# Kernel optimization log

Measured on AMD Instinct MI355X. Metric: run time of the kernel, lower is better.

Reference implementation:

```python
import jax, jax.numpy as jnp
import numpy as np

B, L, C, H = 8, 2048, 512, 8
HD = C // H
MLP_H = int(C * 4.0)
LN_EPS = 1e-5


def _dwconv(x, w, b, groups):
    # x: (B, C, L), w: (C, C//groups, 3), 'same' padding depthwise/grouped conv
    y = jax.lax.conv_general_dilated(
        x, w, window_strides=(1,), padding=((1, 1),),
        feature_group_count=groups,
        dimension_numbers=('NCH', 'OIH', 'NCH'))
    return y + b[None, :, None]


def _ln(x, g, b):
    mu = x.mean(-1, keepdims=True)
    var = ((x - mu) ** 2).mean(-1, keepdims=True)
    return (x - mu) * jax.lax.rsqrt(var + LN_EPS) * g + b


def setup_inputs() -> dict:
    key = jax.random.key(0)
    ks = jax.random.split(key, 32)
    s = 0.02
    d = {
        'x_q': jax.random.normal(ks[0], (B, L, C), jnp.float32),
        'x_kv': jax.random.normal(ks[1], (B, L, C), jnp.float32),
        'cpe1_w': jax.random.normal(ks[2], (C, 1, 3), jnp.float32) * s,
        'cpe1_b': jnp.zeros((C,), jnp.float32),
        'norm1_g': jnp.ones((C,), jnp.float32),
        'norm1_b': jnp.zeros((C,), jnp.float32),
        'in_w': jax.random.normal(ks[3], (C, C), jnp.float32) * s,
        'in_b': jnp.zeros((C,), jnp.float32),
        'act_w': jax.random.normal(ks[4], (C, C), jnp.float32) * s,
        'act_b': jnp.zeros((C,), jnp.float32),
        'dwc_w': jax.random.normal(ks[5], (C, 1, 3), jnp.float32) * s,
        'dwc_b': jnp.zeros((C,), jnp.float32),
        'q_w': jax.random.normal(ks[6], (C, C), jnp.float32) * s,
        'q_b': jnp.zeros((C,), jnp.float32),
        'kv_w': jax.random.normal(ks[7], (C, 2 * C), jnp.float32) * s,
        'kv_b': jnp.zeros((2 * C,), jnp.float32),
        'lepe_w': jax.random.normal(ks[8], (C, 1, 3), jnp.float32) * s,
        'lepe_b': jnp.zeros((C,), jnp.float32),
        'out_w': jax.random.normal(ks[9], (C, C), jnp.float32) * s,
        'out_b': jnp.zeros((C,), jnp.float32),
        'cpe2_w': jax.random.normal(ks[10], (C, 1, 3), jnp.float32) * s,
        'cpe2_b': jnp.zeros((C,), jnp.float32),
        'norm2_g': jnp.ones((C,), jnp.float32),
        'norm2_b': jnp.zeros((C,), jnp.float32),
        'fc1_w': jax.random.normal(ks[11], (C, MLP_H), jnp.float32) * s,
        'fc1_b': jnp.zeros((MLP_H,), jnp.float32),
        'fc2_w': jax.random.normal(ks[12], (MLP_H, C), jnp.float32) * s,
        'fc2_b': jnp.zeros((C,), jnp.float32),
    }
    return d


def _linear_attention(x_q, x_kv, q_w, q_b, kv_w, kv_b, lepe_w, lepe_b):
    b, n, c = x_kv.shape
    kv = x_kv @ kv_w + kv_b                       # (b, n, 2c)
    k, v = kv[..., :c], kv[..., c:]
    q = jax.nn.elu(x_q @ q_w + q_b) + 1.0
    k = jax.nn.elu(k) + 1.0
    # (b, h, n, d)
    q = q.reshape(b, n, H, HD).transpose(0, 2, 1, 3)
    k = k.reshape(b, n, H, HD).transpose(0, 2, 1, 3)
    v = v.reshape(b, n, H, HD).transpose(0, 2, 1, 3)
    k_mean = k.mean(axis=2)                       # (b, h, d)
    z = 1.0 / (jnp.einsum('bhnd,bhd->bhn', q, k_mean) + 1e-6)
    scale = n ** (-0.5)
    kv_mat = jnp.einsum('bhnd,bhne->bhde', k * scale, v * scale)  # (b,h,d,d)
    out = jnp.einsum('bhnd,bhde->bhne', q, kv_mat) * z[..., None]
    out = out.transpose(0, 2, 1, 3).reshape(b, n, c)
    v_flat = v.transpose(0, 2, 1, 3).reshape(b, n, c).transpose(0, 2, 1)  # (b,c,n)
    out = out + _dwconv(v_flat, lepe_w, lepe_b, groups=c).transpose(0, 2, 1)
    return out


def reference(x_q, x_kv, cpe1_w, cpe1_b, norm1_g, norm1_b, in_w, in_b, act_w,
              act_b, dwc_w, dwc_b, q_w, q_b, kv_w, kv_b, lepe_w, lepe_b,
              out_w, out_b, cpe2_w, cpe2_b, norm2_g, norm2_b, fc1_w, fc1_b,
              fc2_w, fc2_b):
    b, l, c = x_kv.shape
    x = x_kv + _dwconv(x_kv.transpose(0, 2, 1), cpe1_w, cpe1_b, c).transpose(0, 2, 1)
    shortcut = x
    x = _ln(x, norm1_g, norm1_b)
    act_res = jax.nn.silu(x @ act_w + act_b)
    # NOTE: torch uses .view(B, C, L): a reshape, not a transpose -- replicate faithfully
    xp = (x @ in_w + in_b).reshape(b, c, l)
    xp = jax.nn.silu(_dwconv(xp, dwc_w, dwc_b, c)).reshape(b, l, c)
    xa = _linear_attention(x_q, xp, q_w, q_b, kv_w, kv_b, lepe_w, lepe_b)
    x = shortcut + ((xa * act_res) @ out_w + out_b)
    x = x + _dwconv(x.transpose(0, 2, 1), cpe2_w, cpe2_b, c).transpose(0, 2, 1)
    h = _ln(x, norm2_g, norm2_b)
    h = jax.nn.gelu(h @ fc1_w + fc1_b, approximate=False) @ fc2_w + fc2_b
    return x + h
```

## Files before the change

kernel.cpp:

```cpp
#include <hip/hip_runtime.h>
#include <cmath>


typedef __bf16 bf16;
typedef __bf16 bf16x8 __attribute__((ext_vector_type(8)));
typedef __bf16 bf16x4 __attribute__((ext_vector_type(4)));
typedef float  f32x4  __attribute__((ext_vector_type(4)));

#define B_  8
#define L_  2048
#define C_  512
#define M_  (B_ * L_)

__device__ __forceinline__ float fastrcp(float x) { return __builtin_amdgcn_rcpf(x); }

__device__ __forceinline__ float siluf(float x)
{
    return x * fastrcp(1.f + __expf(-x));
}
__device__ __forceinline__ float elu1f(float x) { return x > 0.f ? x + 1.f : __expf(x); }

__device__ __forceinline__ float geluf(float x)
{
    const float z = fabsf(x) * 0.70710678118654752f;
    const float t = fastrcp(__builtin_fmaf(z, 0.47047f, 1.f));
    const float poly = t * (0.3480242f + t * (-0.0958798f + t * 0.7478556f));
    const float erfz = __builtin_fmaf(-poly, __expf(-z * z), 1.f);
    const float hx = 0.5f * x;
    return __builtin_fmaf(hx, __builtin_copysignf(erfz, x), hx);
}

__device__ __forceinline__ void load_lds16(const bf16* g, bf16* l)
{
    __builtin_amdgcn_global_load_lds(
        (const __attribute__((address_space(1))) void*)g,
        (__attribute__((address_space(3))) void*)l, 16, 0, 0);
}

__global__ __launch_bounds__(256) void zero_k(float* __restrict__ p, int n)
{
    int i = blockIdx.x * 256 + threadIdx.x;
    if (i < n) p[i] = 0.f;
}

__global__ __launch_bounds__(64) void ws_diag_k(float* __restrict__ out, float v)
{
    if (threadIdx.x == 0 && blockIdx.x == 0) out[0] = v;
}

__global__ __launch_bounds__(256) void f32_to_bf16_k(
    const float* __restrict__ in, bf16* __restrict__ out, int n4)
{
    int i = blockIdx.x * 256 + threadIdx.x;
    if (i >= n4) return;
    float4 v = ((const float4*)in)[i];
    bf16x4 o = { (bf16)v.x, (bf16)v.y, (bf16)v.z, (bf16)v.w };
    ((bf16x4*)out)[i] = o;
}

struct TJob  { const float* W; bf16* Wt; int K; int N; int blk0; };
struct TJobs { TJob j[7]; };

__global__ __launch_bounds__(256) void transpose_all_k(TJobs jobs)
{
    __shared__ float tile[32][33];
    const int bid = blockIdx.x;
    int ji = 0;
#pragma unroll
    for (int i = 1; i < 7; ++i) if (bid >= jobs.j[i].blk0) ji = i;
    const float* W  = jobs.j[ji].W;
    bf16*        Wt = jobs.j[ji].Wt;
    const int K = jobs.j[ji].K, N = jobs.j[ji].N;
    const int rel = bid - jobs.j[ji].blk0;
    const int nb = N >> 5;
    const int n0 = (rel % nb) * 32, k0 = (rel / nb) * 32;
    const int tx = threadIdx.x & 31, ty = threadIdx.x >> 5;
#pragma unroll
    for (int i = 0; i < 32; i += 8)
        tile[ty + i][tx] = W[(size_t)(k0 + ty + i) * N + n0 + tx];
    __syncthreads();
#pragma unroll
    for (int i = 0; i < 32; i += 8)
        Wt[(size_t)(n0 + ty + i) * K + k0 + tx] = (bf16)tile[tx][ty + i];
}

__global__ __launch_bounds__(256) void cpe_ln_k(
    const float* __restrict__ xin, const float* __restrict__ cw,
    const float* __restrict__ cb, const float* __restrict__ g,
    const float* __restrict__ bb, float* __restrict__ xres,
    bf16* __restrict__ xln)
{
    const int token = blockIdx.x;
    const int l = token & (L_ - 1);
    const int tid = threadIdx.x;
    const float* row = xin + (size_t)token * C_;
    float v[2]; float s = 0.f, s2 = 0.f;
#pragma unroll
    for (int i = 0; i < 2; ++i) {
        const int c = tid + i * 256;
        float x0 = row[c];
        float xm = (l > 0)      ? row[c - C_] : 0.f;
        float xp = (l < L_ - 1) ? row[c + C_] : 0.f;
        float t = x0 + xm * cw[3*c] + x0 * cw[3*c+1] + xp * cw[3*c+2] + cb[c];
        v[i] = t; s += t; s2 += t * t;
    }
#pragma unroll
    for (int off = 32; off; off >>= 1) { s += __shfl_down(s, off); s2 += __shfl_down(s2, off); }
    __shared__ float rs[4], rs2[4];
    if ((tid & 63) == 0) { rs[tid >> 6] = s; rs2[tid >> 6] = s2; }
    __syncthreads();
    s  = rs[0] + rs[1] + rs[2] + rs[3];
    s2 = rs2[0] + rs2[1] + rs2[2] + rs2[3];
    const float mu = s * (1.f / C_);
    const float rstd = rsqrtf(s2 * (1.f / C_) - mu * mu + 1e-5f);
    float* orow = xres + (size_t)token * C_;
    bf16*  lrow = xln  + (size_t)token * C_;
#pragma unroll
    for (int i = 0; i < 2; ++i) {
        const int c = tid + i * 256;
        orow[c] = v[i];
        lrow[c] = (bf16)((v[i] - mu) * rstd * g[c] + bb[c]);
    }
}

__global__ __launch_bounds__(256) void dwc_silu_k(
    const bf16* __restrict__ Y, const float* __restrict__ w,
    const float* __restrict__ b, bf16* __restrict__ xp)
{
    const size_t idx = (size_t)blockIdx.x * 256 + threadIdx.x;
    const int m = (int)(idx & (size_t)(L_ * C_ - 1));
    const int ch = m >> 11;
    const int pos = m & (L_ - 1);
    float x0 = (float)Y[idx];
    float xm = (pos > 0)      ? (float)Y[idx - 1] : 0.f;
    float xq = (pos < L_ - 1) ? (float)Y[idx + 1] : 0.f;
    float t = xm * w[3*ch] + x0 * w[3*ch+1] + xq * w[3*ch+2] + b[ch];
    xp[idx] = (bf16)siluf(t);
}

__global__ __launch_bounds__(256) void ksum_k(
    const bf16* __restrict__ kvbT, float* __restrict__ ksum)
{
    const int c = blockIdx.x;
    const int wave = threadIdx.x >> 6, lane = threadIdx.x & 63;
#pragma unroll
    for (int i = 0; i < 2; ++i) {
        const int b = wave + i * 4;
        const bf16* src = kvbT + (size_t)c * M_ + b * L_ + lane * 32;
        float s = 0.f;
#pragma unroll
        for (int u = 0; u < 4; ++u) {
            bf16x8 v = *(const bf16x8*)(src + u * 8);
#pragma unroll
            for (int j = 0; j < 8; ++j) s += (float)v[j];
        }
#pragma unroll
        for (int o = 32; o; o >>= 1) s += __shfl_down(s, o);
        if (lane == 0) ksum[b * C_ + c] = s;
    }
}

__global__ __launch_bounds__(256) void kvmat_mfma_k(
    const bf16* __restrict__ kvbT, float* __restrict__ kvpart)
{
    const int bh = blockIdx.x, b = bh >> 3, h = bh & 7;
    const int tid = threadIdx.x;
    const int wave = tid >> 6, lane = tid & 63;
    const int l16 = lane & 15, quad = lane >> 4;
    __shared__ bf16 As[64 * 72];
    __shared__ bf16 Bs[64 * 72];
    const int r = tid >> 2;
    const int cseg = (tid & 3) * 16;
    const size_t kRow = (size_t)(h * 64 + r) * M_;
    const size_t vRow = (size_t)(512 + h * 64 + r) * M_;

    f32x4 acc[4];
    const f32x4 z4 = { 0.f, 0.f, 0.f, 0.f };
#pragma unroll
    for (int ni = 0; ni < 4; ++ni) acc[ni] = z4;

    for (int it = 0; it < 8; ++it) {
        const size_t colBase = (size_t)b * L_ + blockIdx.y * 512 + it * 64;
        {
            const bf16* ga = kvbT + vRow + colBase + cseg;
            const bf16* gb = kvbT + kRow + colBase + cseg;
            *(uint4*)&As[r * 72 + cseg]     = *(const uint4*)ga;
            *(uint4*)&As[r * 72 + cseg + 8] = *(const uint4*)(ga + 8);
            *(uint4*)&Bs[r * 72 + cseg]     = *(const uint4*)gb;
            *(uint4*)&Bs[r * 72 + cseg + 8] = *(const uint4*)(gb + 8);
        }
        __syncthreads();
#pragma unroll
        for (int kk = 0; kk < 64; kk += 32) {
            bf16x8 af = *(const bf16x8*)(&As[(wave * 16 + l16) * 72 + kk + quad * 8]);
#pragma unroll
            for (int ni = 0; ni < 4; ++ni) {
                bf16x8 bfr = *(const bf16x8*)(&Bs[(ni * 16 + l16) * 72 + kk + quad * 8]);
                acc[ni] = __builtin_amdgcn_mfma_f32_16x16x32_bf16(af, bfr, acc[ni], 0, 0, 0);
            }
        }
        __syncthreads();
    }
    float* dst = kvpart + (size_t)blockIdx.y * 262144 + (size_t)bh * 4096;
#pragma unroll
    for (int ni = 0; ni < 4; ++ni)
#pragma unroll
        for (int rr = 0; rr < 4; ++rr)
            dst[(wave * 16 + quad * 4 + rr) * 64 + ni * 16 + l16] = acc[ni][rr];
}

__global__ __launch_bounds__(256) void kvconv_k(
    const float* __restrict__ p, bf16* __restrict__ out)
{
    int i = blockIdx.x * 256 + threadIdx.x;
    float s = p[i] + p[i + 262144] + p[i + 2 * 262144] + p[i + 3 * 262144];
    out[i] = (bf16)(s * (1.f / (float)L_));
}

__global__ __launch_bounds__(256) void attn_mfma_k(
    const bf16* __restrict__ q, const bf16* __restrict__ kvbT,
    const bf16* __restrict__ kvmatT, const float* __restrict__ ksum,
    const float* __restrict__ lw, const float* __restrict__ lb,
    const bf16* __restrict__ act_res, bf16* __restrict__ xa_mul)
{
    const int bh = blockIdx.x, b = bh >> 3, h = bh & 7;
    const int n0 = blockIdx.y * 64;
    const int tid = threadIdx.x;
    const int wave = tid >> 6, lane = tid & 63;
    const int l16 = lane & 15, quad = lane >> 4;

    __shared__ bf16 kvT[64 * 72];
    __shared__ bf16 kmS[64];

#pragma unroll
    for (int i = 0; i < 2; ++i) {
        const int idx = i * 256 + tid;
        const int row = idx >> 3, col = (idx & 7) * 8;
        *(bf16x8*)&kvT[row * 72 + col] =
            *(const bf16x8*)&kvmatT[(size_t)bh * 4096 + idx * 8];
    }
    if (tid < 64) kmS[tid] = (bf16)(ksum[b * C_ + h * 64 + tid] * (1.f / (float)L_));
    __syncthreads();

    const int tok = n0 + wave * 16;
    const bf16* qbase = q + ((size_t)b * L_ + tok) * C_ + h * 64;
    const bf16x8 af0 = *(const bf16x8*)(qbase + (size_t)l16 * C_ + quad * 8);
    const bf16x8 af1 = *(const bf16x8*)(qbase + (size_t)l16 * C_ + 32 + quad * 8);

    const bf16x8 z8 = { bf16(0.f), bf16(0.f), bf16(0.f), bf16(0.f),
                        bf16(0.f), bf16(0.f), bf16(0.f), bf16(0.f) };
    const bf16x8 km0 = *(const bf16x8*)&kmS[quad * 8];
    const bf16x8 km1 = *(const bf16x8*)&kmS[32 + quad * 8];
    const bf16x8 b20 = (l16 == 0) ? km0 : z8;
    const bf16x8 b21 = (l16 == 0) ? km1 : z8;
    f32x4 zd = { 0.f, 0.f, 0.f, 0.f };
    zd = __builtin_amdgcn_mfma_f32_16x16x32_bf16(af0, b20, zd, 0, 0, 0);
    zd = __builtin_amdgcn_mfma_f32_16x16x32_bf16(af1, b21, zd, 0, 0, 0);
    float zr[4];
#pragma unroll
    for (int r = 0; r < 4; ++r)
        zr[r] = fastrcp(__shfl(zd[r], (lane & 48)) + 1e-6f);

    f32x4 acc[4];
    const f32x4 zf4 = { 0.f, 0.f, 0.f, 0.f };
#pragma unroll
    for (int ni = 0; ni < 4; ++ni) acc[ni] = zf4;
#pragma unroll
    for (int ni = 0; ni < 4; ++ni) {
        const bf16x8 b0 = *(const bf16x8*)&kvT[(ni * 16 + l16) * 72 + quad * 8];
        const bf16x8 b1 = *(const bf16x8*)&kvT[(ni * 16 + l16) * 72 + 32 + quad * 8];
        acc[ni] = __builtin_amdgcn_mfma_f32_16x16x32_bf16(af0, b0, acc[ni], 0, 0, 0);
        acc[ni] = __builtin_amdgcn_mfma_f32_16x16x32_bf16(af1, b1, acc[ni], 0, 0, 0);
    }

#pragma unroll
    for (int ni = 0; ni < 4; ++ni) {
        const int e = ni * 16 + l16;
        const int c = h * 64 + e;
        const float w0 = lw[3*c], w1 = lw[3*c+1], w2 = lw[3*c+2], lbc = lb[c];
        const bf16* vrow = kvbT + (size_t)(512 + c) * M_ + b * L_;
#pragma unroll
        for (int r = 0; r < 4; ++r) {
            const int n = tok + quad * 4 + r;
            const float v0 = (float)vrow[n];
            const float vm = (n > 0)      ? (float)vrow[n - 1] : 0.f;
            const float vp = (n < L_ - 1) ? (float)vrow[n + 1] : 0.f;
            const float lepe = vm * w0 + v0 * w1 + vp * w2 + lbc;
            const float xa = acc[ni][r] * zr[r] + lepe;
            const size_t off = ((size_t)b * L_ + n) * C_ + c;
            xa_mul[off] = (bf16)(xa * (float)act_res[off]);
        }
    }
}

template <int EPI>
__global__ __launch_bounds__(256) void gemm_bt(
    const bf16* __restrict__ A, const bf16* __restrict__ Bt,
    const float* __restrict__ bias, const float* __restrict__ res,
    void* __restrict__ outp, void* __restrict__ outp2, int K, int N)
{
    __shared__ bf16 smem[2 * 128 * 64];
    bf16* As = smem;
    bf16* Bs = smem + 8192;
    const int tid = threadIdx.x;
    const int wave = tid >> 6, lane = tid & 63;
    const int wm = (wave & 1) * 64, wn = (wave >> 1) * 64;
    const int l16 = lane & 15, quad = lane >> 4;
    const size_t tileM = (size_t)blockIdx.x * 128;
    const size_t tileN = (size_t)blockIdx.y * 128;

    const int lrow = lane >> 3;
    const int lcol = (((lane & 7) ^ (lrow & 7))) * 8;
    const int swz  = l16 & 7;

    const f32x4 z4 = { 0.f, 0.f, 0.f, 0.f };
    f32x4 acc[4][4];
#pragma unroll
    for (int mi = 0; mi < 4; ++mi)
#pragma unroll
        for (int ni = 0; ni < 4; ++ni) acc[mi][ni] = z4;

    for (int k0 = 0; k0 < K; k0 += 64) {
#pragma unroll
        for (int it = 0; it < 4; ++it) {
            const int rg = it * 32 + wave * 8;
            load_lds16(A  + (tileM + rg + lrow) * (size_t)K + k0 + lcol, As + rg * 64);
            load_lds16(Bt + (tileN + rg + lrow) * (size_t)K + k0 + lcol, Bs + rg * 64);
        }
        __syncthreads();
#pragma unroll
        for (int kk = 0; kk < 64; kk += 32) {
            bf16x8 af[4], bfr[4];
#pragma unroll
            for (int mi = 0; mi < 4; ++mi)
                af[mi] = *(const bf16x8*)(&As[(wm + mi * 16 + l16) * 64
                                              + ((((kk >> 3) + quad) ^ swz) * 8)]);
#pragma unroll
            for (int ni = 0; ni < 4; ++ni)
                bfr[ni] = *(const bf16x8*)(&Bs[(wn + ni * 16 + l16) * 64
                                               + ((((kk >> 3) + quad) ^ swz) * 8)]);
#pragma unroll
            for (int mi = 0; mi < 4; ++mi)
#pragma unroll
                for (int ni = 0; ni < 4; ++ni)
                    acc[mi][ni] = __builtin_amdgcn_mfma_f32_16x16x32_bf16(
                        af[mi], bfr[ni], acc[mi][ni], 0, 0, 0);
        }
        __syncthreads();
    }

    const int rrow = lane >> 2;
    const int rseg = (lane & 3) * 16;

    if (EPI == 5 || EPI == 7) {
        float* sc = (float*)smem + wave * 1088;
#pragma unroll
        for (int mi = 0; mi < 4; ++mi) {
#pragma unroll
            for (int ni = 0; ni < 4; ++ni)
#pragma unroll
                for (int r = 0; r < 4; ++r)
                    sc[(quad * 4 + r) * 68 + ni * 16 + l16] = acc[mi][ni][r];
            __builtin_amdgcn_sched_barrier(0);
            const size_t rowg = tileM + wm + mi * 16 + rrow;
            const int    colg = (int)tileN + wn + rseg;
            if (EPI == 5) {
                const float* rp = res + rowg * (size_t)N + colg;
                float*       op = (float*)outp + rowg * (size_t)N + colg;
#pragma unroll
                for (int u = 0; u < 4; ++u) {
                    f32x4 v = *(f32x4*)&sc[rrow * 68 + rseg + u * 4];
                    f32x4 rv = *(const f32x4*)(rp + u * 4);
                    f32x4 bv = *(const f32x4*)(bias + colg + u * 4);
                    f32x4 o;
#pragma unroll
                    for (int j = 0; j < 4; ++j) o[j] = v[j] + bv[j] + rv[j];
                    *(f32x4*)(op + u * 4) = o;
                }
            } else {
                const float bv = bias[(int)rowg];
                const bool k_side = (rowg < 512);
                bf16* op = (bf16*)outp + rowg * (size_t)N + colg;
#pragma unroll
                for (int hh = 0; hh < 2; ++hh) {
                    bf16x8 o8;
#pragma unroll
                    for (int j = 0; j < 8; ++j) {
                        float x = sc[rrow * 68 + rseg + hh * 8 + j] + bv;
                        o8[j] = (bf16)(k_side ? elu1f(x) : x);
                    }
                    *(bf16x8*)(op + hh * 8) = o8;
                }
            }
            __builtin_amdgcn_sched_barrier(0);
        }
    } else {
        bf16* sc = (bf16*)smem + wave * 1152;
        float addc[4];
        bool  act_on[4];
#pragma unroll
        for (int ni = 0; ni < 4; ++ni) {
            const int cw = (int)tileN + wn + ni * 16 + l16;
            if (EPI == 8) {
                act_on[ni] = (cw < 512);
                addc[ni] = act_on[ni] ? bias[cw] : res[cw - 512];
            } else { addc[ni] = bias[cw]; act_on[ni] = true; }
        }
#pragma unroll
        for (int mi = 0; mi < 4; ++mi) {
#pragma unroll
            for (int ni = 0; ni < 4; ++ni)
#pragma unroll
                for (int r = 0; r < 4; ++r) {
                    float x = acc[mi][ni][r] + addc[ni];
                    float y;
                    if (EPI == 2)      y = elu1f(x);
                    else if (EPI == 4) y = geluf(x);
                    else               y = act_on[ni] ? siluf(x) : x;
                    sc[(quad * 4 + r) * 72 + ni * 16 + l16] = (bf16)y;
                }
            __builtin_amdgcn_sched_barrier(0);
            const size_t rowg = tileM + wm + mi * 16 + rrow;
            const int    colg = (int)tileN + wn + rseg;
            bf16x8 o0 = *(bf16x8*)&sc[rrow * 72 + rseg];
            bf16x8 o1 = *(bf16x8*)&sc[rrow * 72 + rseg + 8];
            if (EPI == 8) {
                const size_t orow = rowg * (size_t)512;
                bf16* dst = (colg < 512) ? ((bf16*)outp  + orow + colg)
                                         : ((bf16*)outp2 + orow + colg - 512);
                *(bf16x8*)dst = o0; *(bf16x8*)(dst + 8) = o1;
            } else {
                bf16* dst = (bf16*)outp + rowg * (size_t)N + colg;
                *(bf16x8*)dst = o0; *(bf16x8*)(dst + 8) = o1;
            }
            __builtin_amdgcn_sched_barrier(0);
        }
    }
}

template <int EPI>
__global__ __launch_bounds__(512, 2) void gemm8(
    const bf16* __restrict__ A, const bf16* __restrict__ Bt,
    const float* __restrict__ bias, const float* __restrict__ res,
    void* __restrict__ outp, void* __restrict__ outp2, int K, int N)
{
    __shared__ bf16 smem[4 * 256 * 64];
    bf16* const AsBase = smem;
    bf16* const BsBase = smem + 32768;
    const int tid  = threadIdx.x;
    const int wave = tid >> 6, lane = tid & 63;
    const int wrow = wave >> 2, wcol = wave & 3;
    const int l16 = lane & 15, quad = lane >> 4;
    const int lrow = lane >> 3;
    const int lcol = ((lane & 7) ^ lrow) * 8;
    const int swz  = l16 & 7;
    const size_t tileM = (size_t)blockIdx.x * 256;
    const size_t tileN = (size_t)blockIdx.y * 256;

    const bf16* aBase = A  + (tileM + wave * 8 + lrow) * (size_t)K + lcol;
    const bf16* bBase = Bt + (tileN + wave * 8 + lrow) * (size_t)K + lcol;
    const int ldsRow0 = wave * 8;

    f32x4 acc[8][4];
    const f32x4 z4 = { 0.f, 0.f, 0.f, 0.f };
#pragma unroll
    for (int mi = 0; mi < 8; ++mi)
#pragma unroll
        for (int ni = 0; ni < 4; ++ni) acc[mi][ni] = z4;

#pragma unroll
    for (int j = 0; j < 4; ++j) {
        load_lds16(aBase + (size_t)(j * 64) * K, AsBase + (j * 64 + ldsRow0) * 64);
        load_lds16(bBase + (size_t)(j * 64) * K, BsBase + (j * 64 + ldsRow0) * 64);
    }
    asm volatile("s_waitcnt vmcnt(0)" ::: "memory");
    __builtin_amdgcn_s_barrier();

    const int T = K >> 6;
    int cur = 0;
    for (int t = 0; t < T; ++t) {
        const int nxt = cur ^ 1;
        const bool pf = (t + 1 < T);
        const int kc = (t + 1) << 6;
        const bf16* as = AsBase + cur * 16384;
        const bf16* bs = BsBase + cur * 16384;
        bf16* asn = AsBase + nxt * 16384;
        bf16* bsn = BsBase + nxt * 16384;
        bf16x8 af[4][2], bfr[4][2];

#pragma unroll
        for (int j = 0; j < 4; ++j)
#pragma unroll
            for (int kh = 0; kh < 2; ++kh)
                af[j][kh] = *(const bf16x8*)&as[(wrow * 128 + j * 16 + l16) * 64
                                               + (((kh * 4 + quad) ^ swz) * 8)];
#pragma unroll
        for (int ni = 0; ni < 2; ++ni)
#pragma unroll
            for (int kh = 0; kh < 2; ++kh)
                bfr[ni][kh] = *(const bf16x8*)&bs[(wcol * 64 + ni * 16 + l16) * 64
                                                  + (((kh * 4 + quad) ^ swz) * 8)];
        if (pf) {
#pragma unroll
            for (int j = 0; j < 2; ++j) {
                load_lds16(aBase + (size_t)(j * 64) * K + kc, asn + (j * 64 + ldsRow0) * 64);
                load_lds16(bBase + (size_t)(j * 64) * K + kc, bsn + (j * 64 + ldsRow0) * 64);
            }
        }
        __builtin_amdgcn_s_barrier();
        asm volatile("s_waitcnt lgkmcnt(0)" ::: "memory");
        __builtin_amdgcn_sched_barrier(0);
        __builtin_amdgcn_s_setprio(1);
#pragma unroll
        for (int j = 0; j < 4; ++j)
#pragma unroll
            for (int ni = 0; ni < 2; ++ni)
#pragma unroll
                for (int kh = 0; kh < 2; ++kh)
                    acc[j][ni] = __builtin_amdgcn_mfma_f32_16x16x32_bf16(
                        af[j][kh], bfr[ni][kh], acc[j][ni], 0, 0, 0);
        __builtin_amdgcn_s_setprio(0);
        __builtin_amdgcn_s_barrier();

#pragma unroll
        for (int ni = 2; ni < 4; ++ni)
#pragma unroll
            for (int kh = 0; kh < 2; ++kh)
                bfr[ni][kh] = *(const bf16x8*)&bs[(wcol * 64 + ni * 16 + l16) * 64
                                                  + (((kh * 4 + quad) ^ swz) * 8)];
        if (pf) {
#pragma unroll
            for (int j = 2; j < 4; ++j) {
                load_lds16(aBase + (size_t)(j * 64) * K + kc, asn + (j * 64 + ldsRow0) * 64);
                load_lds16(bBase + (size_t)(j * 64) * K + kc, bsn + (j * 64 + ldsRow0) * 64);
            }
        }
        __builtin_amdgcn_s_barrier();
        asm volatile("s_waitcnt lgkmcnt(0)" ::: "memory");
        __builtin_amdgcn_sched_barrier(0);
        __builtin_amdgcn_s_setprio(1);
#pragma unroll
        for (int j = 0; j < 4; ++j)
#pragma unroll
            for (int ni = 2; ni < 4; ++ni)
#pragma unroll
                for (int kh = 0; kh < 2; ++kh)
                    acc[j][ni] = __builtin_amdgcn_mfma_f32_16x16x32_bf16(
                        af[j][kh], bfr[ni][kh], acc[j][ni], 0, 0, 0);
        __builtin_amdgcn_s_setprio(0);
        __builtin_amdgcn_s_barrier();

#pragma unroll
        for (int j = 0; j < 4; ++j)
#pragma unroll
            for (int kh = 0; kh < 2; ++kh)
                af[j][kh] = *(const bf16x8*)&as[(wrow * 128 + 64 + j * 16 + l16) * 64
                                               + (((kh * 4 + quad) ^ swz) * 8)];
        __builtin_amdgcn_s_barrier();
        asm volatile("s_waitcnt lgkmcnt(0)" ::: "memory");
        __builtin_amdgcn_sched_barrier(0);
        __builtin_amdgcn_s_setprio(1);
#pragma unroll
        for (int j = 0; j < 4; ++j)
#pragma unroll
            for (int ni = 0; ni < 2; ++ni)
#pragma unroll
                for (int kh = 0; kh < 2; ++kh)
                    acc[4 + j][ni] = __builtin_amdgcn_mfma_f32_16x16x32_bf16(
                        af[j][kh], bfr[ni][kh], acc[4 + j][ni], 0, 0, 0);
        __builtin_amdgcn_s_setprio(0);
        __builtin_amdgcn_s_barrier();

        if (pf) asm volatile("s_waitcnt vmcnt(0)" ::: "memory");
        __builtin_amdgcn_s_barrier();
        __builtin_amdgcn_sched_barrier(0);
        __builtin_amdgcn_s_setprio(1);
#pragma unroll
        for (int j = 0; j < 4; ++j)
#pragma unroll
            for (int ni = 2; ni < 4; ++ni)
#pragma unroll
                for (int kh = 0; kh < 2; ++kh)
                    acc[4 + j][ni] = __builtin_amdgcn_mfma_f32_16x16x32_bf16(
                        af[j][kh], bfr[ni][kh], acc[4 + j][ni], 0, 0, 0);
        __builtin_amdgcn_s_setprio(0);
        __builtin_amdgcn_s_barrier();

        cur = nxt;
    }

    const int rrow = lane >> 2;
    const int rseg = (lane & 3) * 16;

    if (EPI == 5 || EPI == 7) {
        float* sc = (float*)smem + wave * 1088;
#pragma unroll
        for (int mi = 0; mi < 8; ++mi) {
#pragma unroll
            for (int ni = 0; ni < 4; ++ni)
#pragma unroll
                for (int r = 0; r < 4; ++r)
                    sc[(quad * 4 + r) * 68 + ni * 16 + l16] = acc[mi][ni][r];
            __builtin_amdgcn_sched_barrier(0);
            const size_t rowg = tileM + wrow * 128 + mi * 16 + rrow;
            const int    colg = (int)tileN + wcol * 64 + rseg;
            if (EPI == 5) {
                const float* rp = res + rowg * (size_t)N + colg;
                float*       op = (float*)outp + rowg * (size_t)N + colg;
#pragma unroll
                for (int u = 0; u < 4; ++u) {
                    f32x4 v = *(f32x4*)&sc[rrow * 68 + rseg + u * 4];
                    f32x4 rv = *(const f32x4*)(rp + u * 4);
                    f32x4 bv = *(const f32x4*)(bias + colg + u * 4);
                    f32x4 o;
#pragma unroll
                    for (int j = 0; j < 4; ++j) o[j] = v[j] + bv[j] + rv[j];
                    *(f32x4*)(op + u * 4) = o;
                }
            } else {
                const float bv = bias[(int)rowg];
                const bool k_side = (rowg < 512);
                bf16* op = (bf16*)outp + rowg * (size_t)N + colg;
#pragma unroll
                for (int hh = 0; hh < 2; ++hh) {
                    bf16x8 o8;
#pragma unroll
                    for (int j = 0; j < 8; ++j) {
                        float x = sc[rrow * 68 + rseg + hh * 8 + j] + bv;
                        o8[j] = (bf16)(k_side ? elu1f(x) : x);
                    }
                    *(bf16x8*)(op + hh * 8) = o8;
                }
            }
            __builtin_amdgcn_sched_barrier(0);
        }
    } else {
        bf16* sc = (bf16*)smem + wave * 1152;
        float addc[4];
        bool  act_on[4];
#pragma unroll
        for (int ni = 0; ni < 4; ++ni) {
            const int cw = (int)tileN + wcol * 64 + ni * 16 + l16;
            if (EPI == 8) {
                act_on[ni] = (cw < 512);
                addc[ni] = act_on[ni] ? bias[cw] : res[cw - 512];
            } else { addc[ni] = bias[cw]; act_on[ni] = true; }
        }
#pragma unroll
        for (int mi = 0; mi < 8; ++mi) {
#pragma unroll
            for (int ni = 0; ni < 4; ++ni)
#pragma unroll
                for (int r = 0; r < 4; ++r) {
                    float x = acc[mi][ni][r] + addc[ni];
                    float y;
                    if (EPI == 2)      y = elu1f(x);
                    else if (EPI == 4) y = geluf(x);
                    else               y = act_on[ni] ? siluf(x) : x;
                    sc[(quad * 4 + r) * 72 + ni * 16 + l16] = (bf16)y;
                }
            __builtin_amdgcn_sched_barrier(0);
            const size_t rowg = tileM + wrow * 128 + mi * 16 + rrow;
            const int    colg = (int)tileN + wcol * 64 + rseg;
            bf16x8 o0 = *(bf16x8*)&sc[rrow * 72 + rseg];
            bf16x8 o1 = *(bf16x8*)&sc[rrow * 72 + rseg + 8];
            if (EPI == 8) {
                const size_t orow = rowg * (size_t)512;
                bf16* dst = (colg < 512) ? ((bf16*)outp  + orow + colg)
                                         : ((bf16*)outp2 + orow + colg - 512);
                *(bf16x8*)dst = o0; *(bf16x8*)(dst + 8) = o1;
            } else {
                bf16* dst = (bf16*)outp + rowg * (size_t)N + colg;
                *(bf16x8*)dst = o0; *(bf16x8*)(dst + 8) = o1;
            }
            __builtin_amdgcn_sched_barrier(0);
        }
    }
}

#define OFF_WT_ACTIN ((size_t)0)
#define OFF_WT_Q    ((size_t)1048576)
#define OFF_WT_KV   ((size_t)1572864)
#define OFF_WT_OUT  ((size_t)2621440)
#define OFF_WT_FC1  ((size_t)3145728)
#define OFF_WT_FC2  ((size_t)5242880)
#define OFF_XLN     ((size_t)7340032)
#define OFF_ACTRES  ((size_t)24117248)
#define OFF_Y       ((size_t)40894464)
#define OFF_XP      ((size_t)57671680)
#define OFF_KV      ((size_t)74448896)
#define OFF_KSUM    ((size_t)108003328)
#define OFF_XAMUL   ((size_t)109068288)
#define OFF_X3      ((size_t)24117248)
#define OFF_H1      ((size_t)57671680)
#define WS_REQUIRED ((size_t)125845504)

extern "C" void kernel_launch(void* const* d_in, const int* in_sizes, int n_in,
                              void* d_out, int out_size, void* d_ws, size_t ws_size,
                              hipStream_t stream)
{
    const float* x_q    = (const float*)d_in[0];
    const float* x_kv   = (const float*)d_in[1];
    const float* cpe1_w = (const float*)d_in[2];
    const float* cpe1_b = (const float*)d_in[3];
    const float* n1_g   = (const float*)d_in[4];
    const float* n1_b   = (const float*)d_in[5];
    const float* in_w   = (const float*)d_in[6];
    const float* in_b   = (const float*)d_in[7];
    const float* act_w  = (const float*)d_in[8];
    const float* act_b  = (const float*)d_in[9];
    const float* dwc_w  = (const float*)d_in[10];
    const float* dwc_b  = (const float*)d_in[11];
    const float* q_w    = (const float*)d_in[12];
    const float* q_b    = (const float*)d_in[13];
    const float* kv_w   = (const float*)d_in[14];
    const float* kv_b   = (const float*)d_in[15];
    const float* lepe_w = (const float*)d_in[16];
    const float* lepe_b = (const float*)d_in[17];
    const float* out_w  = (const float*)d_in[18];
    const float* out_b  = (const float*)d_in[19];
    const float* cpe2_w = (const float*)d_in[20];
    const float* cpe2_b = (const float*)d_in[21];
    const float* n2_g   = (const float*)d_in[22];
    const float* n2_b   = (const float*)d_in[23];
    const float* fc1_w  = (const float*)d_in[24];
    const float* fc1_b  = (const float*)d_in[25];
    const float* fc2_w  = (const float*)d_in[26];
    const float* fc2_b  = (const float*)d_in[27];

    float* outf = (float*)d_out;

    if (ws_size < WS_REQUIRED) {
        zero_k<<<(out_size + 255) / 256, 256, 0, stream>>>(outf, out_size);
        ws_diag_k<<<1, 64, 0, stream>>>(outf, (float)ws_size);
        return;
    }

    char* ws = (char*)d_ws;
    bf16*  wt_actin = (bf16*)(ws + OFF_WT_ACTIN);
    bf16*  wt_q   = (bf16*)(ws + OFF_WT_Q);
    bf16*  wt_kv  = (bf16*)(ws + OFF_WT_KV);
    bf16*  wt_out = (bf16*)(ws + OFF_WT_OUT);
    bf16*  wt_fc1 = (bf16*)(ws + OFF_WT_FC1);
    bf16*  wt_fc2 = (bf16*)(ws + OFF_WT_FC2);
    bf16*  xln    = (bf16*)(ws + OFF_XLN);
    bf16*  xqb    = (bf16*)(ws + OFF_XLN);
    bf16*  kvbf   = (bf16*)(ws + OFF_XLN);
    bf16*  hln    = (bf16*)(ws + OFF_XLN);
    bf16*  actres = (bf16*)(ws + OFF_ACTRES);
    bf16*  Y      = (bf16*)(ws + OFF_Y);
    bf16*  qb     = (bf16*)(ws + OFF_Y);
    bf16*  xp     = (bf16*)(ws + OFF_XP);
    float* kvpart = (float*)(ws + OFF_XP);
    bf16*  kvbT   = (bf16*)(ws + OFF_KV);
    float* ksum   = (float*)(ws + OFF_KSUM);
    bf16*  xamul  = (bf16*)(ws + OFF_XAMUL);
    float* x3     = (float*)(ws + OFF_X3);
    bf16*  h1     = (bf16*)(ws + OFF_H1);

    TJobs jobs;
    jobs.j[0] = { act_w, wt_actin,             512,  512,    0 };
    jobs.j[1] = { in_w,  wt_actin + 512 * 512, 512,  512,  256 };
    jobs.j[2] = { q_w,   wt_q,                 512,  512,  512 };
    jobs.j[3] = { kv_w,  wt_kv,                512, 1024,  768 };
    jobs.j[4] = { out_w, wt_out,               512,  512, 1280 };
    jobs.j[5] = { fc1_w, wt_fc1,               512, 2048, 1536 };
    jobs.j[6] = { fc2_w, wt_fc2,              2048,  512, 2560 };
    transpose_all_k<<<3584, 256, 0, stream>>>(jobs);

    cpe_ln_k<<<M_, 256, 0, stream>>>(x_kv, cpe1_w, cpe1_b, n1_g, n1_b, outf, xln);

    gemm8<8><<<dim3(64, 4), 512, 0, stream>>>(xln, wt_actin, act_b, in_b, actres, Y, 512, 1024);

    dwc_silu_k<<<32768, 256, 0, stream>>>(Y, dwc_w, dwc_b, xp);

    f32_to_bf16_k<<<8192, 256, 0, stream>>>(x_q, xqb, M_ * C_ / 4);
    gemm_bt<2><<<dim3(128, 4), 256, 0, stream>>>(xqb, wt_q, q_b, nullptr, qb, nullptr, 512, 512);

    gemm8<7><<<dim3(4, 64), 512, 0, stream>>>(wt_kv, xp, kv_b, nullptr, kvbT, nullptr, 512, M_);

    ksum_k<<<C_, 256, 0, stream>>>(kvbT, ksum);
    kvmat_mfma_k<<<dim3(64, 4), 256, 0, stream>>>(kvbT, kvpart);
    kvconv_k<<<1024, 256, 0, stream>>>(kvpart, kvbf);

    attn_mfma_k<<<dim3(64, 32), 256, 0, stream>>>(qb, kvbT, kvbf, ksum,
                                                  lepe_w, lepe_b, actres, xamul);

    gemm_bt<5><<<dim3(128, 4), 256, 0, stream>>>(xamul, wt_out, out_b, outf, outf, nullptr, 512, 512);

    cpe_ln_k<<<M_, 256, 0, stream>>>(outf, cpe2_w, cpe2_b, n2_g, n2_b, x3, hln);

    gemm8<4><<<dim3(64, 8), 512, 0, stream>>>(hln, wt_fc1, fc1_b, nullptr, h1, nullptr, 512, 2048);
    gemm_bt<5><<<dim3(128, 4),  256, 0, stream>>>(h1,  wt_fc2, fc2_b, x3, outf, nullptr, 2048, 512);

    (void)in_sizes; (void)n_in; (void)out_size; (void)ws_size;
}
```

Before: 469.3 us.

## Fuse x_q cast into transpose, vectorize dwconv, swizzle and simplify GEMM epilogues

```diff
diff --git a/kernel.cpp b/kernel.cpp
--- a/kernel.cpp
+++ b/kernel.cpp
@@ -48,23 +48,21 @@
     if (threadIdx.x == 0 && blockIdx.x == 0) out[0] = v;
 }
 
-__global__ __launch_bounds__(256) void f32_to_bf16_k(
-    const float* __restrict__ in, bf16* __restrict__ out, int n4)
-{
-    int i = blockIdx.x * 256 + threadIdx.x;
-    if (i >= n4) return;
-    float4 v = ((const float4*)in)[i];
-    bf16x4 o = { (bf16)v.x, (bf16)v.y, (bf16)v.z, (bf16)v.w };
-    ((bf16x4*)out)[i] = o;
-}
-
 struct TJob  { const float* W; bf16* Wt; int K; int N; int blk0; };
 struct TJobs { TJob j[7]; };
 
-__global__ __launch_bounds__(256) void transpose_all_k(TJobs jobs)
-{
+__global__ __launch_bounds__(256) void transpose_all_k(
+    TJobs jobs, const float* __restrict__ xq, bf16* __restrict__ xqb)
+{
+    const int bid = blockIdx.x;
+    if (bid >= 3584) {
+        const int i = (bid - 3584) * 256 + threadIdx.x;
+        float4 v = ((const float4*)xq)[i];
+        bf16x4 o = { (bf16)v.x, (bf16)v.y, (bf16)v.z, (bf16)v.w };
+        ((bf16x4*)xqb)[i] = o;
+        return;
+    }
     __shared__ float tile[32][33];
-    const int bid = blockIdx.x;
     int ji = 0;
 #pragma unroll
     for (int i = 1; i < 7; ++i) if (bid >= jobs.j[i].blk0) ji = i;
@@ -127,15 +125,23 @@
     const bf16* __restrict__ Y, const float* __restrict__ w,
     const float* __restrict__ b, bf16* __restrict__ xp)
 {
-    const size_t idx = (size_t)blockIdx.x * 256 + threadIdx.x;
+    const size_t idx = ((size_t)blockIdx.x * 256 + threadIdx.x) * 8;
     const int m = (int)(idx & (size_t)(L_ * C_ - 1));
     const int ch = m >> 11;
     const int pos = m & (L_ - 1);
-    float x0 = (float)Y[idx];
-    float xm = (pos > 0)      ? (float)Y[idx - 1] : 0.f;
-    float xq = (pos < L_ - 1) ? (float)Y[idx + 1] : 0.f;
-    float t = xm * w[3*ch] + x0 * w[3*ch+1] + xq * w[3*ch+2] + b[ch];
-    xp[idx] = (bf16)siluf(t);
+    const bf16x8 c = *(const bf16x8*)(Y + idx);
+    const float left  = (pos > 0)      ? (float)Y[idx - 1] : 0.f;
+    const float right = (pos + 8 < L_) ? (float)Y[idx + 8] : 0.f;
+    const float w0 = w[3*ch], w1 = w[3*ch+1], w2 = w[3*ch+2], bc = b[ch];
+    bf16x8 o;
+#pragma unroll
+    for (int j = 0; j < 8; ++j) {
+        const float x0 = (float)c[j];
+        const float xm = j ? (float)c[j-1] : left;
+        const float xq = (j < 7) ? (float)c[j+1] : right;
+        o[j] = (bf16)siluf(xm * w0 + x0 * w1 + xq * w2 + bc);
+    }
+    *(bf16x8*)(xp + idx) = o;
 }
 
 __global__ __launch_bounds__(256) void ksum_k(
@@ -396,6 +402,9 @@
         }
     } else {
         bf16* sc = (bf16*)smem + wave * 1152;
+        const int wrot = (quad >> 1) * 16;
+        const int rrot = ((rrow >> 3) & 1) * 16;
+        const int cbase = (rseg + rrot) & 63;
         float addc[4];
         bool  act_on[4];
 #pragma unroll
@@ -417,13 +426,13 @@
                     if (EPI == 2)      y = elu1f(x);
                     else if (EPI == 4) y = geluf(x);
                     else               y = act_on[ni] ? siluf(x) : x;
-                    sc[(quad * 4 + r) * 72 + ni * 16 + l16] = (bf16)y;
+                    sc[(quad * 4 + r) * 72 + ((ni * 16 + l16 + wrot) & 63)] = (bf16)y;
                 }
             __builtin_amdgcn_sched_barrier(0);
             const size_t rowg = tileM + wm + mi * 16 + rrow;
             const int    colg = (int)tileN + wn + rseg;
-            bf16x8 o0 = *(bf16x8*)&sc[rrow * 72 + rseg];
-            bf16x8 o1 = *(bf16x8*)&sc[rrow * 72 + rseg + 8];
+            bf16x8 o0 = *(bf16x8*)&sc[rrow * 72 + cbase];
+            bf16x8 o1 = *(bf16x8*)&sc[rrow * 72 + cbase + 8];
             if (EPI == 8) {
                 const size_t orow = rowg * (size_t)512;
                 bf16* dst = (colg < 512) ? ((bf16*)outp  + orow + colg)
@@ -589,91 +598,28 @@
         cur = nxt;
     }
 
-    const int rrow = lane >> 2;
-    const int rseg = (lane & 3) * 16;
-
-    if (EPI == 5 || EPI == 7) {
-        float* sc = (float*)smem + wave * 1088;
-#pragma unroll
-        for (int mi = 0; mi < 8; ++mi) {
-#pragma unroll
-            for (int ni = 0; ni < 4; ++ni)
-#pragma unroll
-                for (int r = 0; r < 4; ++r)
-                    sc[(quad * 4 + r) * 68 + ni * 16 + l16] = acc[mi][ni][r];
-            __builtin_amdgcn_sched_barrier(0);
-            const size_t rowg = tileM + wrow * 128 + mi * 16 + rrow;
-            const int    colg = (int)tileN + wcol * 64 + rseg;
-            if (EPI == 5) {
-                const float* rp = res + rowg * (size_t)N + colg;
-                float*       op = (float*)outp + rowg * (size_t)N + colg;
-#pragma unroll
-                for (int u = 0; u < 4; ++u) {
-                    f32x4 v = *(f32x4*)&sc[rrow * 68 + rseg + u * 4];
-                    f32x4 rv = *(const f32x4*)(rp + u * 4);
-                    f32x4 bv = *(const f32x4*)(bias + colg + u * 4);
-                    f32x4 o;
-#pragma unroll
-                    for (int j = 0; j < 4; ++j) o[j] = v[j] + bv[j] + rv[j];
-                    *(f32x4*)(op + u * 4) = o;
-                }
-            } else {
-                const float bv = bias[(int)rowg];
-                const bool k_side = (rowg < 512);
-                bf16* op = (bf16*)outp + rowg * (size_t)N + colg;
-#pragma unroll
-                for (int hh = 0; hh < 2; ++hh) {
-                    bf16x8 o8;
-#pragma unroll
-                    for (int j = 0; j < 8; ++j) {
-                        float x = sc[rrow * 68 + rseg + hh * 8 + j] + bv;
-                        o8[j] = (bf16)(k_side ? elu1f(x) : x);
-                    }
-                    *(bf16x8*)(op + hh * 8) = o8;
+#pragma unroll
+    for (int mi = 0; mi < 8; ++mi) {
+#pragma unroll
+        for (int ni = 0; ni < 4; ++ni) {
+#pragma unroll
+            for (int r = 0; r < 4; ++r) {
+                const size_t row = tileM + wrow * 128 + mi * 16 + quad * 4 + r;
+                const int   col = (int)tileN + wcol * 64 + ni * 16 + l16;
+                float v = acc[mi][ni][r];
+                const size_t oidx = row * (size_t)N + col;
+                if (EPI == 2)      ((bf16*)outp)[oidx] = (bf16)elu1f(v + bias[col]);
+                else if (EPI == 4) ((bf16*)outp)[oidx] = (bf16)geluf(v + bias[col]);
+                else if (EPI == 5) ((float*)outp)[oidx] = v + bias[col] + res[oidx];
+                else if (EPI == 7) {
+                    v += bias[(int)row];
+                    ((bf16*)outp)[oidx] = (bf16)((row < 512) ? elu1f(v) : v);
+                } else if (EPI == 8) {
+                    const size_t orow = row * (size_t)512;
+                    if (col < 512) ((bf16*)outp )[orow + col]       = (bf16)siluf(v + bias[col]);
+                    else           ((bf16*)outp2)[orow + col - 512] = (bf16)(v + res[col - 512]);
                 }
             }
-            __builtin_amdgcn_sched_barrier(0);
-        }
-    } else {
-        bf16* sc = (bf16*)smem + wave * 1152;
-        float addc[4];
-        bool  act_on[4];
-#pragma unroll
-        for (int ni = 0; ni < 4; ++ni) {
-            const int cw = (int)tileN + wcol * 64 + ni * 16 + l16;
-            if (EPI == 8) {
-                act_on[ni] = (cw < 512);
-                addc[ni] = act_on[ni] ? bias[cw] : res[cw - 512];
-            } else { addc[ni] = bias[cw]; act_on[ni] = true; }
-        }
-#pragma unroll
-        for (int mi = 0; mi < 8; ++mi) {
-#pragma unroll
-            for (int ni = 0; ni < 4; ++ni)
-#pragma unroll
-                for (int r = 0; r < 4; ++r) {
-                    float x = acc[mi][ni][r] + addc[ni];
-                    float y;
-                    if (EPI == 2)      y = elu1f(x);
-                    else if (EPI == 4) y = geluf(x);
-                    else               y = act_on[ni] ? siluf(x) : x;
-                    sc[(quad * 4 + r) * 72 + ni * 16 + l16] = (bf16)y;
-                }
-            __builtin_amdgcn_sched_barrier(0);
-            const size_t rowg = tileM + wrow * 128 + mi * 16 + rrow;
-            const int    colg = (int)tileN + wcol * 64 + rseg;
-            bf16x8 o0 = *(bf16x8*)&sc[rrow * 72 + rseg];
-            bf16x8 o1 = *(bf16x8*)&sc[rrow * 72 + rseg + 8];
-            if (EPI == 8) {
-                const size_t orow = rowg * (size_t)512;
-                bf16* dst = (colg < 512) ? ((bf16*)outp  + orow + colg)
-                                         : ((bf16*)outp2 + orow + colg - 512);
-                *(bf16x8*)dst = o0; *(bf16x8*)(dst + 8) = o1;
-            } else {
-                bf16* dst = (bf16*)outp + rowg * (size_t)N + colg;
-                *(bf16x8*)dst = o0; *(bf16x8*)(dst + 8) = o1;
-            }
-            __builtin_amdgcn_sched_barrier(0);
         }
     }
 }
@@ -744,7 +690,6 @@
     bf16*  wt_fc1 = (bf16*)(ws + OFF_WT_FC1);
     bf16*  wt_fc2 = (bf16*)(ws + OFF_WT_FC2);
     bf16*  xln    = (bf16*)(ws + OFF_XLN);
-    bf16*  xqb    = (bf16*)(ws + OFF_XLN);
     bf16*  kvbf   = (bf16*)(ws + OFF_XLN);
     bf16*  hln    = (bf16*)(ws + OFF_XLN);
     bf16*  actres = (bf16*)(ws + OFF_ACTRES);
@@ -754,6 +699,7 @@
     float* kvpart = (float*)(ws + OFF_XP);
     bf16*  kvbT   = (bf16*)(ws + OFF_KV);
     float* ksum   = (float*)(ws + OFF_KSUM);
+    bf16*  xqb    = (bf16*)(ws + OFF_XAMUL);
     bf16*  xamul  = (bf16*)(ws + OFF_XAMUL);
     float* x3     = (float*)(ws + OFF_X3);
     bf16*  h1     = (bf16*)(ws + OFF_H1);
@@ -766,15 +712,14 @@
     jobs.j[4] = { out_w, wt_out,               512,  512, 1280 };
     jobs.j[5] = { fc1_w, wt_fc1,               512, 2048, 1536 };
     jobs.j[6] = { fc2_w, wt_fc2,              2048,  512, 2560 };
-    transpose_all_k<<<3584, 256, 0, stream>>>(jobs);
+    transpose_all_k<<<11776, 256, 0, stream>>>(jobs, x_q, xqb);
 
     cpe_ln_k<<<M_, 256, 0, stream>>>(x_kv, cpe1_w, cpe1_b, n1_g, n1_b, outf, xln);
 
     gemm8<8><<<dim3(64, 4), 512, 0, stream>>>(xln, wt_actin, act_b, in_b, actres, Y, 512, 1024);
 
-    dwc_silu_k<<<32768, 256, 0, stream>>>(Y, dwc_w, dwc_b, xp);
-
-    f32_to_bf16_k<<<8192, 256, 0, stream>>>(x_q, xqb, M_ * C_ / 4);
+    dwc_silu_k<<<4096, 256, 0, stream>>>(Y, dwc_w, dwc_b, xp);
+
     gemm_bt<2><<<dim3(128, 4), 256, 0, stream>>>(xqb, wt_q, q_b, nullptr, qb, nullptr, 512, 512);
 
     gemm8<7><<<dim3(4, 64), 512, 0, stream>>>(wt_kv, xp, kv_b, nullptr, kvbT, nullptr, 512, M_);
```

Measured after the change: 538.2 us. 1.15x slower.
